# Performance work log

Measured on AMD Instinct MI355X. Metric: run time of the kernel, lower is better.

## Reference

```python
import jax, jax.numpy as jnp
import numpy as np

DIM, HEADS, WS, SS = 256, 8, 4, 2
B, D, H, W = 2, 16, 56, 56


def _rel_pos_index(ws):
    coords = np.stack(np.meshgrid(np.arange(ws), np.arange(ws), np.arange(ws), indexing='ij'))
    flat = coords.reshape(3, -1)                      # [3, n]
    rel = (flat[:, :, None] - flat[:, None, :]).transpose(1, 2, 0).astype(np.int64)  # [n,n,3]
    rel[..., 0] += ws - 1; rel[..., 1] += ws - 1; rel[..., 2] += ws - 1
    rel[..., 0] *= (2 * ws - 1) ** 2
    rel[..., 1] *= (2 * ws - 1)
    return rel.sum(-1)                                # [n, n]


def _attn_mask(d, h, w, ws, ss):
    # dims are divisible by ws here, so padded dims == dims (matches torch ceil-pad)
    img = np.zeros((d, h, w))
    sl = (slice(0, -ws), slice(-ws, -ss), slice(-ss, None))
    cnt = 0
    for dsl in sl:
        for hsl in sl:
            for wsl in sl:
                img[dsl, hsl, wsl] = cnt
                cnt += 1
    mw = img.reshape(d // ws, ws, h // ws, ws, w // ws, ws)
    mw = mw.transpose(0, 2, 4, 1, 3, 5).reshape(-1, ws ** 3)   # [nW, n]
    diff = mw[:, None, :] - mw[:, :, None]
    return np.where(diff != 0, -100.0, 0.0).astype(np.float32)  # [nW, n, n]


def _window_partition(x, ws):
    b, d, h, w, c = x.shape
    x = x.reshape(b, d // ws, ws, h // ws, ws, w // ws, ws, c)
    return x.transpose(0, 1, 3, 5, 2, 4, 6, 7).reshape(-1, ws ** 3, c)


def _window_reverse(win, ws, b, d, h, w, c):
    x = win.reshape(b, d // ws, h // ws, w // ws, ws, ws, ws, c)
    return x.transpose(0, 1, 4, 2, 5, 3, 6, 7).reshape(b, d, h, w, c)


def _ln(x, g, b, eps=1e-5):
    mu = x.mean(-1, keepdims=True)
    var = ((x - mu) ** 2).mean(-1, keepdims=True)
    return (x - mu) * jax.lax.rsqrt(var + eps) * g + b


def setup_inputs() -> dict:
    key = jax.random.key(0)
    ks = jax.random.split(key, 8)
    s = 0.02
    return {
        'x': jax.random.normal(ks[0], (B, D, H, W, DIM), jnp.float32),
        'norm1_g': jnp.ones((DIM,), jnp.float32),
        'norm1_b': jnp.zeros((DIM,), jnp.float32),
        'qkv_w': jax.random.normal(ks[1], (DIM, 3 * DIM), jnp.float32) * s,
        'qkv_b': jnp.zeros((3 * DIM,), jnp.float32),
        'proj_w': jax.random.normal(ks[2], (DIM, DIM), jnp.float32) * s,
        'proj_b': jnp.zeros((DIM,), jnp.float32),
        'rpb_table': jax.random.normal(ks[3], ((2 * WS - 1) ** 3, HEADS), jnp.float32) * s,
        'norm2_g': jnp.ones((DIM,), jnp.float32),
        'norm2_b': jnp.zeros((DIM,), jnp.float32),
        'fc1_w': jax.random.normal(ks[4], (DIM, 4 * DIM), jnp.float32) * s,
        'fc1_b': jnp.zeros((4 * DIM,), jnp.float32),
        'fc2_w': jax.random.normal(ks[5], (4 * DIM, DIM), jnp.float32) * s,
        'fc2_b': jnp.zeros((DIM,), jnp.float32),
    }


def reference(x, norm1_g, norm1_b, qkv_w, qkv_b, proj_w, proj_b, rpb_table,
              norm2_g, norm2_b, fc1_w, fc1_b, fc2_w, fc2_b):
    b, d, h, w, c = x.shape
    nh, ws, ss = HEADS, WS, SS
    hd = c // nh
    shortcut = x

    xn = _ln(x, norm1_g, norm1_b)
    xs = jnp.roll(xn, shift=(-ss, -ss, -ss), axis=(1, 2, 3))
    xw = _window_partition(xs, ws)            # [B_, n, c]
    B_, n, _ = xw.shape

    qkv = (xw @ qkv_w + qkv_b).reshape(B_, n, 3, nh, hd).transpose(2, 0, 3, 1, 4)
    q, k, v = qkv[0], qkv[1], qkv[2]          # [B_, nh, n, hd]
    attn = jnp.einsum('bhqd,bhkd->bhqk', q * (hd ** -0.5), k)

    rpi = jnp.asarray(_rel_pos_index(ws).reshape(-1))
    bias = rpb_table[rpi].reshape(n, n, nh).transpose(2, 0, 1)  # [nh, n, n]
    attn = attn + bias[None]

    mask = jnp.asarray(_attn_mask(d, h, w, ws, ss))             # [nW, n, n]
    nW = mask.shape[0]
    attn = attn.reshape(B_ // nW, nW, nh, n, n) + mask[None, :, None]
    attn = jax.nn.softmax(attn.reshape(B_, nh, n, n), axis=-1)

    out = jnp.einsum('bhqk,bhkd->bhqd', attn, v).transpose(0, 2, 1, 3).reshape(B_, n, c)
    out = out @ proj_w + proj_b

    xr = _window_reverse(out, ws, b, d, h, w, c)
    xr = jnp.roll(xr, shift=(ss, ss, ss), axis=(1, 2, 3))
    x1 = shortcut + xr

    y = _ln(x1, norm2_g, norm2_b)
    y = jax.nn.gelu(y @ fc1_w + fc1_b, approximate=False) @ fc2_w + fc2_b
    return x1 + y
```

## Files before the change

### kernel.cpp

```cpp
#include <hip/hip_runtime.h>
#include <math.h>


using f32x4  = __attribute__((ext_vector_type(4))) float;
using bf16x8 = __attribute__((ext_vector_type(8))) short;

#define M_CHUNK 25088
#define W_CHUNK 392
#define NCHUNK  4

__device__ __forceinline__ short f2bf(float f) {
  unsigned u = __builtin_bit_cast(unsigned, f);
  u += 0x7fffu + ((u >> 16) & 1u);
  return (short)(u >> 16);
}
__device__ __forceinline__ float bf2f(short s) {
  return __builtin_bit_cast(float, ((unsigned)(unsigned short)s) << 16);
}

__global__ void cast_transpose_k(const float* __restrict__ in,
                                 short* __restrict__ out, int K, int N) {
  const int idx = blockIdx.x * 256 + threadIdx.x;
  const int k = idx / N, n = idx % N;
  out[(size_t)n * K + k] = f2bf(in[idx]);
}

__global__ __launch_bounds__(256) void ln1_part_k(
    const float* __restrict__ x, const float* __restrict__ g,
    const float* __restrict__ bta, short* __restrict__ xw, int row0) {
  const int wave = threadIdx.x >> 6, lane = threadIdx.x & 63;
  const int lr = blockIdx.x * 4 + wave;
  const int row = row0 + lr;
  const int win = row >> 6, tok = row & 63;
  const int b = win / 784, wi = win % 784;
  const int wd = wi / 196, wh = (wi / 14) % 14, ww = wi % 14;
  const int tz = tok >> 4, ty = (tok >> 2) & 3, tx = tok & 3;
  const int gd = (wd * 4 + tz + 2) & 15;
  int gh = wh * 4 + ty + 2; if (gh >= 56) gh -= 56;
  int gw = ww * 4 + tx + 2; if (gw >= 56) gw -= 56;
  const size_t src = ((((size_t)b * 16 + gd) * 56 + gh) * 56 + gw) * 256;
  const float4 v = ((const float4*)(x + src))[lane];
  float s = v.x + v.y + v.z + v.w;
#pragma unroll
  for (int m = 1; m < 64; m <<= 1) s += __shfl_xor(s, m);
  const float mean = s * (1.f / 256.f);
  const float dx = v.x - mean, dy = v.y - mean, dz = v.z - mean, dw = v.w - mean;
  float q = dx * dx + dy * dy + dz * dz + dw * dw;
#pragma unroll
  for (int m = 1; m < 64; m <<= 1) q += __shfl_xor(q, m);
  const float rstd = rsqrtf(q * (1.f / 256.f) + 1e-5f);
  const float4 gg = ((const float4*)g)[lane];
  const float4 bb = ((const float4*)bta)[lane];
  short4 o;
  o.x = f2bf(dx * rstd * gg.x + bb.x);
  o.y = f2bf(dy * rstd * gg.y + bb.y);
  o.z = f2bf(dz * rstd * gg.z + bb.z);
  o.w = f2bf(dw * rstd * gg.w + bb.w);
  *(short4*)(xw + (size_t)lr * 256 + lane * 4) = o;
}

__global__ __launch_bounds__(256) void ln2_k(
    const float* __restrict__ x1, const float* __restrict__ g,
    const float* __restrict__ bta, short* __restrict__ yn, int row0) {
  const int wave = threadIdx.x >> 6, lane = threadIdx.x & 63;
  const int lr = blockIdx.x * 4 + wave;
  const float4 v = ((const float4*)(x1 + (size_t)(row0 + lr) * 256))[lane];
  float s = v.x + v.y + v.z + v.w;
#pragma unroll
  for (int m = 1; m < 64; m <<= 1) s += __shfl_xor(s, m);
  const float mean = s * (1.f / 256.f);
  const float dx = v.x - mean, dy = v.y - mean, dz = v.z - mean, dw = v.w - mean;
  float q = dx * dx + dy * dy + dz * dz + dw * dw;
#pragma unroll
  for (int m = 1; m < 64; m <<= 1) q += __shfl_xor(q, m);
  const float rstd = rsqrtf(q * (1.f / 256.f) + 1e-5f);
  const float4 gg = ((const float4*)g)[lane];
  const float4 bb = ((const float4*)bta)[lane];
  short4 o;
  o.x = f2bf(dx * rstd * gg.x + bb.x);
  o.y = f2bf(dy * rstd * gg.y + bb.y);
  o.z = f2bf(dz * rstd * gg.z + bb.z);
  o.w = f2bf(dw * rstd * gg.w + bb.w);
  *(short4*)(yn + (size_t)lr * 256 + lane * 4) = o;
}

template <int EPI>
__global__ __launch_bounds__(256) void gemm_k(
    const short* __restrict__ A, const short* __restrict__ Bt,
    const float* __restrict__ bias, const void* __restrict__ resid,
    void* __restrict__ OutP, int N, int K, int row0) {
  __shared__ short As[128 * 72];
  __shared__ short Bs[128 * 72];
  const int tid = threadIdx.x;
  const int wave = tid >> 6, lane = tid & 63;
  const int quad = lane >> 4, l15 = lane & 15;
  const int m0 = blockIdx.y * 128;
  const int n0 = blockIdx.x * 128;
  const int wm = (wave >> 1) * 64, wn = (wave & 1) * 64;
  const int p_base = wave * 256;

  f32x4 acc[4][4] = {};

  for (int k0 = 0; k0 < K; k0 += 64) {
    bf16x8 va[4], vb[4];
#pragma unroll
    for (int i = 0; i < 4; ++i) {
      const int p = p_base + i * 64 + lane;
      const int row = p >> 3, c = p & 7;
      va[i] = *(const bf16x8*)(A  + (size_t)(m0 + row) * K + (k0 + c * 8));
      vb[i] = *(const bf16x8*)(Bt + (size_t)(n0 + row) * K + (k0 + c * 8));
    }
    __syncthreads();
#pragma unroll
    for (int i = 0; i < 4; ++i) {
      const int p = p_base + i * 64 + lane;
      const int row = p >> 3, c = p & 7;
      *(bf16x8*)(As + row * 72 + c * 8) = va[i];
      *(bf16x8*)(Bs + row * 72 + c * 8) = vb[i];
    }
    __syncthreads();
#pragma unroll
    for (int ks = 0; ks < 2; ++ks) {
      bf16x8 af[4], bfr[4];
#pragma unroll
      for (int t = 0; t < 4; ++t) {
        af[t]  = *(const bf16x8*)(As + (wm + t * 16 + l15) * 72 + (ks * 4 + quad) * 8);
        bfr[t] = *(const bf16x8*)(Bs + (wn + t * 16 + l15) * 72 + (ks * 4 + quad) * 8);
      }
#pragma unroll
      for (int mt = 0; mt < 4; ++mt)
#pragma unroll
        for (int nt = 0; nt < 4; ++nt)
          acc[mt][nt] = __builtin_amdgcn_mfma_f32_16x16x32_bf16(
              af[mt], bfr[nt], acc[mt][nt], 0, 0, 0);
    }
  }

  if constexpr (EPI == 0 || EPI == 1) {
    short* out = (short*)OutP;
#pragma unroll
    for (int nt = 0; nt < 4; ++nt) {
      const int col = n0 + wn + nt * 16 + l15;
      const float bv = bias[col];
#pragma unroll
      for (int mt = 0; mt < 4; ++mt)
#pragma unroll
        for (int reg = 0; reg < 4; ++reg) {
          const int row = m0 + wm + mt * 16 + quad * 4 + reg;
          float v = acc[mt][nt][reg] + bv;
          if constexpr (EPI == 1)
            v = 0.5f * v * (1.f + erff(v * 0.70710678118654752f));
          out[(size_t)row * N + col] = f2bf(v);
        }
    }
  } else if constexpr (EPI == 2) {
    float* out = (float*)OutP;
    const float* rs = (const float*)resid;
#pragma unroll
    for (int nt = 0; nt < 4; ++nt) {
      const int col = n0 + wn + nt * 16 + l15;
      const float bv = bias[col];
#pragma unroll
      for (int mt = 0; mt < 4; ++mt)
#pragma unroll
        for (int reg = 0; reg < 4; ++reg) {
          const int row = row0 + m0 + wm + mt * 16 + quad * 4 + reg;
          const int win = row >> 6, tok = row & 63;
          const int b = win / 784, wi = win % 784;
          const int wd = wi / 196, wh = (wi / 14) % 14, ww = wi % 14;
          const int tz = tok >> 4, ty = (tok >> 2) & 3, tx = tok & 3;
          const int gd = (wd * 4 + tz + 2) & 15;
          int gh = wh * 4 + ty + 2; if (gh >= 56) gh -= 56;
          int gw = ww * 4 + tx + 2; if (gw >= 56) gw -= 56;
          const size_t dst =
              ((((size_t)b * 16 + gd) * 56 + gh) * 56 + gw) * 256 + col;
          out[dst] = rs[dst] + acc[mt][nt][reg] + bv;
        }
    }
  } else {
    float* out = (float*)OutP;
    const float* rs = (const float*)resid;
#pragma unroll
    for (int nt = 0; nt < 4; ++nt) {
      const int col = n0 + wn + nt * 16 + l15;
      const float bv = bias[col];
#pragma unroll
      for (int mt = 0; mt < 4; ++mt)
#pragma unroll
        for (int reg = 0; reg < 4; ++reg) {
          const int row = m0 + wm + mt * 16 + quad * 4 + reg;
          const float v = rs[(size_t)row * 256 + col] +
                          acc[mt][nt][reg] + bv;
          out[(size_t)row * 256 + col] = v;
        }
    }
  }
}

__global__ __launch_bounds__(256) void attn_k(
    const short* __restrict__ qkv, const float* __restrict__ rpb,
    short* __restrict__ aout, int win0) {
  __shared__ short Plds[4 * 64 * 80];
  const int tid = threadIdx.x;
  const int wave = tid >> 6, lane = tid & 63;
  const int quad = lane >> 4, l15 = lane & 15;
  const int wl = blockIdx.x >> 1;
  const int h = ((blockIdx.x & 1) << 2) + wave;
  const int wi = (win0 + wl) % 784;
  const int wd = wi / 196, wh = (wi / 14) % 14, ww = wi % 14;
  const short* base = qkv + (size_t)wl * (64 * 768);

  bf16x8 qf[4], kf[4];
#pragma unroll
  for (int t = 0; t < 4; ++t) {
    const short* qp = base + (size_t)(t * 16 + l15) * 768 + h * 32 + quad * 8;
    qf[t] = *(const bf16x8*)qp;
    kf[t] = *(const bf16x8*)(qp + 256);
  }
  f32x4 S[4][4] = {};
#pragma unroll
  for (int mt = 0; mt < 4; ++mt)
#pragma unroll
    for (int nt = 0; nt < 4; ++nt)
      S[mt][nt] = __builtin_amdgcn_mfma_f32_16x16x32_bf16(
          qf[mt], kf[nt], S[mt][nt], 0, 0, 0);

  const bool bd = (wd == 3), bh = (wh == 13), bw = (ww == 13);
  const int yc = l15 >> 2, xc = l15 & 3;
  int labc[4];
#pragma unroll
  for (int nt = 0; nt < 4; ++nt) {
    const int rd = bd ? (nt < 2 ? 1 : 2) : 0;
    const int rh = bh ? (yc < 2 ? 1 : 2) : 0;
    const int rw = bw ? (xc < 2 ? 1 : 2) : 0;
    labc[nt] = rd * 9 + rh * 3 + rw;
  }
  const float scale = 0.17677669529663687f;
#pragma unroll
  for (int mt = 0; mt < 4; ++mt) {
    const int rdr = bd ? (mt < 2 ? 1 : 2) : 0;
    const int rhr = bh ? (quad < 2 ? 1 : 2) : 0;
#pragma unroll
    for (int reg = 0; reg < 4; ++reg) {
      const int rwr = bw ? (reg < 2 ? 1 : 2) : 0;
      const int labr = rdr * 9 + rhr * 3 + rwr;
      float sc[4];
#pragma unroll
      for (int nt = 0; nt < 4; ++nt) {
        const int rpi = (mt - nt + 3) * 49 + (quad - yc + 3) * 7 + (reg - xc + 3);
        const float bias = rpb[rpi * 8 + h];
        const float mv = (labr == labc[nt]) ? 0.f : -100.f;
        sc[nt] = S[mt][nt][reg] * scale + bias + mv;
      }
      float mx = fmaxf(fmaxf(sc[0], sc[1]), fmaxf(sc[2], sc[3]));
      mx = fmaxf(mx, __shfl_xor(mx, 1));
      mx = fmaxf(mx, __shfl_xor(mx, 2));
      mx = fmaxf(mx, __shfl_xor(mx, 4));
      mx = fmaxf(mx, __shfl_xor(mx, 8));
      float p[4], sum = 0.f;
#pragma unroll
      for (int nt = 0; nt < 4; ++nt) { p[nt] = __expf(sc[nt] - mx); sum += p[nt]; }
      sum += __shfl_xor(sum, 1);
      sum += __shfl_xor(sum, 2);
      sum += __shfl_xor(sum, 4);
      sum += __shfl_xor(sum, 8);
      const float inv = 1.f / sum;
      const int r = mt * 16 + quad * 4 + reg;
#pragma unroll
      for (int nt = 0; nt < 4; ++nt)
        Plds[(wave * 64 + r) * 80 + nt * 16 + l15] = f2bf(p[nt] * inv);
    }
  }

  bf16x8 vf[2][2];
#pragma unroll
  for (int kt = 0; kt < 2; ++kt)
#pragma unroll
    for (int n2 = 0; n2 < 2; ++n2)
#pragma unroll
      for (int j = 0; j < 8; ++j)
        vf[kt][n2][j] =
            base[(size_t)(kt * 32 + quad * 8 + j) * 768 + 512 + h * 32 + n2 * 16 + l15];

  f32x4 O[4][2] = {};
#pragma unroll
  for (int mt = 0; mt < 4; ++mt) {
    const short* pr = &Plds[(wave * 64 + mt * 16 + l15) * 80 + quad * 8];
    const bf16x8 pa0 = *(const bf16x8*)pr;
    const bf16x8 pa1 = *(const bf16x8*)(pr + 32);
#pragma unroll
    for (int n2 = 0; n2 < 2; ++n2) {
      O[mt][n2] = __builtin_amdgcn_mfma_f32_16x16x32_bf16(pa0, vf[0][n2], O[mt][n2], 0, 0, 0);
      O[mt][n2] = __builtin_amdgcn_mfma_f32_16x16x32_bf16(pa1, vf[1][n2], O[mt][n2], 0, 0, 0);
    }
  }
#pragma unroll
  for (int mt = 0; mt < 4; ++mt)
#pragma unroll
    for (int n2 = 0; n2 < 2; ++n2)
#pragma unroll
      for (int reg = 0; reg < 4; ++reg) {
        const int tok = mt * 16 + quad * 4 + reg;
        aout[((size_t)wl * 64 + tok) * 256 + h * 32 + n2 * 16 + l15] =
            f2bf(O[mt][n2][reg]);
      }
}

extern "C" void kernel_launch(void* const* d_in, const int* in_sizes, int n_in,
                              void* d_out, int out_size, void* d_ws,
                              size_t ws_size, hipStream_t stream) {
  const float* x      = (const float*)d_in[0];
  const float* n1g    = (const float*)d_in[1];
  const float* n1b    = (const float*)d_in[2];
  const float* qkv_w  = (const float*)d_in[3];
  const float* qkv_b  = (const float*)d_in[4];
  const float* proj_w = (const float*)d_in[5];
  const float* proj_b = (const float*)d_in[6];
  const float* rpb    = (const float*)d_in[7];
  const float* n2g    = (const float*)d_in[8];
  const float* n2b    = (const float*)d_in[9];
  const float* fc1_w  = (const float*)d_in[10];
  const float* fc1_b  = (const float*)d_in[11];
  const float* fc2_w  = (const float*)d_in[12];
  const float* fc2_b  = (const float*)d_in[13];

  char* ws = (char*)d_ws;
  short* wt_qkv  = (short*)(ws + 0);
  short* wt_proj = (short*)(ws + 393216);
  short* wt_fc1  = (short*)(ws + 524288);
  short* wt_fc2  = (short*)(ws + 1048576);
  short* bufS    = (short*)(ws + 1572864);
  short* bufL    = (short*)(ws + 14417920);
  float* x1      = (float*)d_out;

  cast_transpose_k<<<768, 256, 0, stream>>>(qkv_w, wt_qkv, 256, 768);
  cast_transpose_k<<<256, 256, 0, stream>>>(proj_w, wt_proj, 256, 256);
  cast_transpose_k<<<1024, 256, 0, stream>>>(fc1_w, wt_fc1, 256, 1024);
  cast_transpose_k<<<1024, 256, 0, stream>>>(fc2_w, wt_fc2, 1024, 256);

  for (int c = 0; c < NCHUNK; ++c) {
    const int row0 = c * M_CHUNK, win0 = c * W_CHUNK;
    ln1_part_k<<<M_CHUNK / 4, 256, 0, stream>>>(x, n1g, n1b, bufS, row0);
    gemm_k<0><<<dim3(6, M_CHUNK / 128), 256, 0, stream>>>(
        bufS, wt_qkv, qkv_b, nullptr, bufL, 768, 256, 0);
    attn_k<<<W_CHUNK * 2, 256, 0, stream>>>(bufL, rpb, bufS, win0);
    gemm_k<2><<<dim3(2, M_CHUNK / 128), 256, 0, stream>>>(
        bufS, wt_proj, proj_b, x, x1, 256, 256, row0);
  }
  for (int c = 0; c < NCHUNK; ++c) {
    const int row0 = c * M_CHUNK;
    ln2_k<<<M_CHUNK / 4, 256, 0, stream>>>(x1, n2g, n2b, bufS, row0);
    gemm_k<1><<<dim3(8, M_CHUNK / 128), 256, 0, stream>>>(
        bufS, wt_fc1, fc1_b, nullptr, bufL, 1024, 256, 0);
    gemm_k<3><<<dim3(2, M_CHUNK / 128), 256, 0, stream>>>(
        bufL, wt_fc2, fc2_b, x1 + (size_t)row0 * 256,
        x1 + (size_t)row0 * 256, 256, 1024, 0);
  }
}
```

Baseline: 820.0 us.

## Drop row chunking, merge weight transposes, use direct global-to-LDS loads with XOR swizzle

Removes the four-way M chunking so each stage runs as a single full-size launch, and merges the four weight cast-transpose launches into one. The GEMM tile loads now go straight from global memory to LDS via global_load_lds, replacing the register round trip. The LDS tile uses an XOR column swizzle instead of row padding to avoid bank conflicts. This cuts launch count and staging overhead, but needs a much larger workspace for the full-size intermediates and loses the cache locality that per-chunk processing gave.

```diff
diff --git a/kernel.cpp b/kernel.cpp
--- a/kernel.cpp
+++ b/kernel.cpp
@@ -4,33 +4,41 @@
 
 using f32x4  = __attribute__((ext_vector_type(4))) float;
 using bf16x8 = __attribute__((ext_vector_type(8))) short;
-
-#define M_CHUNK 25088
-#define W_CHUNK 392
-#define NCHUNK  4
 
 __device__ __forceinline__ short f2bf(float f) {
   unsigned u = __builtin_bit_cast(unsigned, f);
   u += 0x7fffu + ((u >> 16) & 1u);
   return (short)(u >> 16);
 }
-__device__ __forceinline__ float bf2f(short s) {
-  return __builtin_bit_cast(float, ((unsigned)(unsigned short)s) << 16);
-}
-
-__global__ void cast_transpose_k(const float* __restrict__ in,
-                                 short* __restrict__ out, int K, int N) {
-  const int idx = blockIdx.x * 256 + threadIdx.x;
+
+#define GLDS16(g, l) __builtin_amdgcn_global_load_lds(                        \
+    (__attribute__((address_space(1))) void*)(g),                             \
+    (__attribute__((address_space(3))) void*)(l), 16, 0, 0)
+
+__global__ void transpose_all_k(const float* __restrict__ qkv_w,
+                                const float* __restrict__ proj_w,
+                                const float* __restrict__ fc1_w,
+                                const float* __restrict__ fc2_w,
+                                short* __restrict__ o_qkv,
+                                short* __restrict__ o_proj,
+                                short* __restrict__ o_fc1,
+                                short* __restrict__ o_fc2) {
+  int bid = blockIdx.x;
+  const float* in; short* out; int K, N;
+  if (bid < 768)       { in = qkv_w;  out = o_qkv;  K = 256;  N = 768; }
+  else if (bid < 1024) { in = proj_w; out = o_proj; K = 256;  N = 256;  bid -= 768; }
+  else if (bid < 2048) { in = fc1_w;  out = o_fc1;  K = 256;  N = 1024; bid -= 1024; }
+  else                 { in = fc2_w;  out = o_fc2;  K = 1024; N = 256;  bid -= 2048; }
+  const int idx = bid * 256 + threadIdx.x;
   const int k = idx / N, n = idx % N;
   out[(size_t)n * K + k] = f2bf(in[idx]);
 }
 
 __global__ __launch_bounds__(256) void ln1_part_k(
     const float* __restrict__ x, const float* __restrict__ g,
-    const float* __restrict__ bta, short* __restrict__ xw, int row0) {
+    const float* __restrict__ bta, short* __restrict__ xw) {
   const int wave = threadIdx.x >> 6, lane = threadIdx.x & 63;
-  const int lr = blockIdx.x * 4 + wave;
-  const int row = row0 + lr;
+  const int row = blockIdx.x * 4 + wave;
   const int win = row >> 6, tok = row & 63;
   const int b = win / 784, wi = win % 784;
   const int wd = wi / 196, wh = (wi / 14) % 14, ww = wi % 14;
@@ -56,15 +64,15 @@
   o.y = f2bf(dy * rstd * gg.y + bb.y);
   o.z = f2bf(dz * rstd * gg.z + bb.z);
   o.w = f2bf(dw * rstd * gg.w + bb.w);
-  *(short4*)(xw + (size_t)lr * 256 + lane * 4) = o;
+  *(short4*)(xw + (size_t)row * 256 + lane * 4) = o;
 }
 
 __global__ __launch_bounds__(256) void ln2_k(
     const float* __restrict__ x1, const float* __restrict__ g,
-    const float* __restrict__ bta, short* __restrict__ yn, int row0) {
+    const float* __restrict__ bta, short* __restrict__ yn) {
   const int wave = threadIdx.x >> 6, lane = threadIdx.x & 63;
-  const int lr = blockIdx.x * 4 + wave;
-  const float4 v = ((const float4*)(x1 + (size_t)(row0 + lr) * 256))[lane];
+  const int row = blockIdx.x * 4 + wave;
+  const float4 v = ((const float4*)(x1 + (size_t)row * 256))[lane];
   float s = v.x + v.y + v.z + v.w;
 #pragma unroll
   for (int m = 1; m < 64; m <<= 1) s += __shfl_xor(s, m);
@@ -81,42 +89,36 @@
   o.y = f2bf(dy * rstd * gg.y + bb.y);
   o.z = f2bf(dz * rstd * gg.z + bb.z);
   o.w = f2bf(dw * rstd * gg.w + bb.w);
-  *(short4*)(yn + (size_t)lr * 256 + lane * 4) = o;
+  *(short4*)(yn + (size_t)row * 256 + lane * 4) = o;
 }
 
 template <int EPI>
 __global__ __launch_bounds__(256) void gemm_k(
     const short* __restrict__ A, const short* __restrict__ Bt,
-    const float* __restrict__ bias, const void* __restrict__ resid,
-    void* __restrict__ OutP, int N, int K, int row0) {
-  __shared__ short As[128 * 72];
-  __shared__ short Bs[128 * 72];
+    const float* __restrict__ bias, const float* __restrict__ resid,
+    void* __restrict__ OutP, int N, int K) {
+  __shared__ short As[128 * 64];
+  __shared__ short Bs[128 * 64];
   const int tid = threadIdx.x;
   const int wave = tid >> 6, lane = tid & 63;
   const int quad = lane >> 4, l15 = lane & 15;
   const int m0 = blockIdx.y * 128;
   const int n0 = blockIdx.x * 128;
   const int wm = (wave >> 1) * 64, wn = (wave & 1) * 64;
-  const int p_base = wave * 256;
 
   f32x4 acc[4][4] = {};
 
   for (int k0 = 0; k0 < K; k0 += 64) {
-    bf16x8 va[4], vb[4];
+    __syncthreads();
 #pragma unroll
     for (int i = 0; i < 4; ++i) {
-      const int p = p_base + i * 64 + lane;
-      const int row = p >> 3, c = p & 7;
-      va[i] = *(const bf16x8*)(A  + (size_t)(m0 + row) * K + (k0 + c * 8));
-      vb[i] = *(const bf16x8*)(Bt + (size_t)(n0 + row) * K + (k0 + c * 8));
-    }
-    __syncthreads();
-#pragma unroll
-    for (int i = 0; i < 4; ++i) {
-      const int p = p_base + i * 64 + lane;
-      const int row = p >> 3, c = p & 7;
-      *(bf16x8*)(As + row * 72 + c * 8) = va[i];
-      *(bf16x8*)(Bs + row * 72 + c * 8) = vb[i];
+      const int p = wave * 256 + i * 64 + lane;
+      const int row = p >> 3;
+      const int c = (p & 7) ^ (row & 7);
+      GLDS16(A  + (size_t)(m0 + row) * K + (k0 + c * 8),
+             As + (size_t)(wave * 256 + i * 64) * 8);
+      GLDS16(Bt + (size_t)(n0 + row) * K + (k0 + c * 8),
+             Bs + (size_t)(wave * 256 + i * 64) * 8);
     }
     __syncthreads();
 #pragma unroll
@@ -124,8 +126,12 @@
       bf16x8 af[4], bfr[4];
 #pragma unroll
       for (int t = 0; t < 4; ++t) {
-        af[t]  = *(const bf16x8*)(As + (wm + t * 16 + l15) * 72 + (ks * 4 + quad) * 8);
-        bfr[t] = *(const bf16x8*)(Bs + (wn + t * 16 + l15) * 72 + (ks * 4 + quad) * 8);
+        const int ra = wm + t * 16 + l15;
+        const int ca = (ks * 4 + quad) ^ (ra & 7);
+        af[t] = *(const bf16x8*)(As + ra * 64 + ca * 8);
+        const int rb = wn + t * 16 + l15;
+        const int cb = (ks * 4 + quad) ^ (rb & 7);
+        bfr[t] = *(const bf16x8*)(Bs + rb * 64 + cb * 8);
       }
 #pragma unroll
       for (int mt = 0; mt < 4; ++mt)
@@ -155,7 +161,6 @@
     }
   } else if constexpr (EPI == 2) {
     float* out = (float*)OutP;
-    const float* rs = (const float*)resid;
 #pragma unroll
     for (int nt = 0; nt < 4; ++nt) {
       const int col = n0 + wn + nt * 16 + l15;
@@ -164,7 +169,7 @@
       for (int mt = 0; mt < 4; ++mt)
 #pragma unroll
         for (int reg = 0; reg < 4; ++reg) {
-          const int row = row0 + m0 + wm + mt * 16 + quad * 4 + reg;
+          const int row = m0 + wm + mt * 16 + quad * 4 + reg;
           const int win = row >> 6, tok = row & 63;
           const int b = win / 784, wi = win % 784;
           const int wd = wi / 196, wh = (wi / 14) % 14, ww = wi % 14;
@@ -174,12 +179,11 @@
           int gw = ww * 4 + tx + 2; if (gw >= 56) gw -= 56;
           const size_t dst =
               ((((size_t)b * 16 + gd) * 56 + gh) * 56 + gw) * 256 + col;
-          out[dst] = rs[dst] + acc[mt][nt][reg] + bv;
+          out[dst] = resid[dst] + acc[mt][nt][reg] + bv;
         }
     }
   } else {
     float* out = (float*)OutP;
-    const float* rs = (const float*)resid;
 #pragma unroll
     for (int nt = 0; nt < 4; ++nt) {
       const int col = n0 + wn + nt * 16 + l15;
@@ -189,9 +193,8 @@
 #pragma unroll
         for (int reg = 0; reg < 4; ++reg) {
           const int row = m0 + wm + mt * 16 + quad * 4 + reg;
-          const float v = rs[(size_t)row * 256 + col] +
-                          acc[mt][nt][reg] + bv;
-          out[(size_t)row * 256 + col] = v;
+          out[(size_t)row * 256 + col] =
+              resid[(size_t)row * 256 + col] + acc[mt][nt][reg] + bv;
         }
     }
   }
@@ -199,16 +202,16 @@
 
 __global__ __launch_bounds__(256) void attn_k(
     const short* __restrict__ qkv, const float* __restrict__ rpb,
-    short* __restrict__ aout, int win0) {
+    short* __restrict__ aout) {
   __shared__ short Plds[4 * 64 * 80];
   const int tid = threadIdx.x;
   const int wave = tid >> 6, lane = tid & 63;
   const int quad = lane >> 4, l15 = lane & 15;
-  const int wl = blockIdx.x >> 1;
+  const int win = blockIdx.x >> 1;
   const int h = ((blockIdx.x & 1) << 2) + wave;
-  const int wi = (win0 + wl) % 784;
+  const int wi = win % 784;
   const int wd = wi / 196, wh = (wi / 14) % 14, ww = wi % 14;
-  const short* base = qkv + (size_t)wl * (64 * 768);
+  const short* base = qkv + (size_t)win * (64 * 768);
 
   bf16x8 qf[4], kf[4];
 #pragma unroll
@@ -301,7 +304,7 @@
 #pragma unroll
       for (int reg = 0; reg < 4; ++reg) {
         const int tok = mt * 16 + quad * 4 + reg;
-        aout[((size_t)wl * 64 + tok) * 256 + h * 32 + n2 * 16 + l15] =
+        aout[((size_t)win * 64 + tok) * 256 + h * 32 + n2 * 16 + l15] =
             f2bf(O[mt][n2][reg]);
       }
 }
@@ -330,30 +333,20 @@
   short* wt_fc1  = (short*)(ws + 524288);
   short* wt_fc2  = (short*)(ws + 1048576);
   short* bufS    = (short*)(ws + 1572864);
-  short* bufL    = (short*)(ws + 14417920);
+  short* bufL    = (short*)(ws + 52953088);
   float* x1      = (float*)d_out;
 
-  cast_transpose_k<<<768, 256, 0, stream>>>(qkv_w, wt_qkv, 256, 768);
-  cast_transpose_k<<<256, 256, 0, stream>>>(proj_w, wt_proj, 256, 256);
-  cast_transpose_k<<<1024, 256, 0, stream>>>(fc1_w, wt_fc1, 256, 1024);
-  cast_transpose_k<<<1024, 256, 0, stream>>>(fc2_w, wt_fc2, 1024, 256);
-
-  for (int c = 0; c < NCHUNK; ++c) {
-    const int row0 = c * M_CHUNK, win0 = c * W_CHUNK;
-    ln1_part_k<<<M_CHUNK / 4, 256, 0, stream>>>(x, n1g, n1b, bufS, row0);
-    gemm_k<0><<<dim3(6, M_CHUNK / 128), 256, 0, stream>>>(
-        bufS, wt_qkv, qkv_b, nullptr, bufL, 768, 256, 0);
-    attn_k<<<W_CHUNK * 2, 256, 0, stream>>>(bufL, rpb, bufS, win0);
-    gemm_k<2><<<dim3(2, M_CHUNK / 128), 256, 0, stream>>>(
-        bufS, wt_proj, proj_b, x, x1, 256, 256, row0);
-  }
-  for (int c = 0; c < NCHUNK; ++c) {
-    const int row0 = c * M_CHUNK;
-    ln2_k<<<M_CHUNK / 4, 256, 0, stream>>>(x1, n2g, n2b, bufS, row0);
-    gemm_k<1><<<dim3(8, M_CHUNK / 128), 256, 0, stream>>>(
-        bufS, wt_fc1, fc1_b, nullptr, bufL, 1024, 256, 0);
-    gemm_k<3><<<dim3(2, M_CHUNK / 128), 256, 0, stream>>>(
-        bufL, wt_fc2, fc2_b, x1 + (size_t)row0 * 256,
-        x1 + (size_t)row0 * 256, 256, 1024, 0);
-  }
-}
+  transpose_all_k<<<3072, 256, 0, stream>>>(qkv_w, proj_w, fc1_w, fc2_w,
+                                            wt_qkv, wt_proj, wt_fc1, wt_fc2);
+  ln1_part_k<<<25088, 256, 0, stream>>>(x, n1g, n1b, bufS);
+  gemm_k<0><<<dim3(6, 784), 256, 0, stream>>>(bufS, wt_qkv, qkv_b, nullptr,
+                                              bufL, 768, 256);
+  attn_k<<<3136, 256, 0, stream>>>(bufL, rpb, bufS);
+  gemm_k<2><<<dim3(2, 784), 256, 0, stream>>>(bufS, wt_proj, proj_b, x,
+                                              x1, 256, 256);
+  ln2_k<<<25088, 256, 0, stream>>>(x1, n2g, n2b, bufS);
+  gemm_k<1><<<dim3(8, 784), 256, 0, stream>>>(bufS, wt_fc1, fc1_b, nullptr,
+                                              bufL, 1024, 256);
+  gemm_k<3><<<dim3(2, 784), 256, 0, stream>>>(bufL, wt_fc2, fc2_b, x1,
+                                              x1, 256, 1024);
+}
```

Result: faster. 732.2 us (-10.7%).
